# Kernel tuning notes

Hardware: AMD Instinct MI355X
Metric: run time of the kernel (lower is better)

## Reference

```python
import jax, jax.numpy as jnp
import numpy as np

# ---- constants mirroring the torch module ----
OSAMP = 8            # temporal oversampling factor
MAX_ITER = 10        # forward solver iterations (LBFGS replaced by fixed GD)
NEG_SHIFT = 2 * OSAMP
OTP = 5              # baseline frames subtracted from ctc/aif
C_SHARP = 500.0      # sharpness constant C=500 in fermi_ir_func
LR = 0.1             # fixed step size for the deterministic forward solve


def interp_linear_1d(x, size):
    # interp_linear_1D: linear upsampling along last (time) axis
    return jax.image.resize(x, x.shape[:-1] + (size,), method='linear')


def fermi_ir(eta, t_os):
    # eta: [B,3,H,W] = (amplitude A, decay rate k, delay t0); t_os: [Tos]
    tsh = t_os - t_os[NEG_SHIFT]                    # negative time shift
    A = eta[:, 0][..., None]                        # [B,H,W,1]
    k = eta[:, 1][..., None]
    t0 = eta[:, 2][..., None]
    step = jax.nn.sigmoid(C_SHARP * tsh)            # sharp causal onset (C=500)
    return A * jax.nn.sigmoid(k * (t0 - tsh)) * step  # [B,H,W,Tos]


def convolve(aif, ir):
    # linear convolution along time via FFT; output aligned with neg_shift offset
    Tos = ir.shape[-1]
    n = 2 * Tos
    Fa = jnp.fft.rfft(aif, n=n, axis=-1)            # [B,1,1,n/2+1]
    Fi = jnp.fft.rfft(ir, n=n, axis=-1)             # [B,H,W,n/2+1]
    full = jnp.fft.irfft(Fa * Fi, n=n, axis=-1)
    return jax.lax.dynamic_slice_in_dim(full, NEG_SHIFT, Tos, axis=-1)


def make_objective(ctc, aif, time, eta_prior, lambda_reg):
    # preprocessing from FermiDataConsLBFGS.forward
    aif = aif - aif[..., :OTP].mean(-1, keepdims=True)
    ctc = ctc - ctc[..., :OTP].mean(-1, keepdims=True)
    Tos = OSAMP * ctc.shape[-1]
    aif_os = interp_linear_1d(aif, Tos)
    ctc_os = interp_linear_1d(ctc, Tos)
    t_os = interp_linear_1d(time, Tos)
    ctc_dc = ctc_os[..., ::OSAMP]                   # [B,H,W,T]
    C_nn = (eta_prior ** 2).sum(axis=(0, 2, 3), keepdims=True)  # [1,3,1,1]
    C_dc = (ctc_dc ** 2).sum()
    sp_lam = jax.nn.softplus(lambda_reg).squeeze()

    def F_obj(eta):  # FermiDConsObj.__call__ (OD disabled: indx_dc = all frames)
        ir = fermi_ir(eta, t_os)
        ctc_est = convolve(aif_os, ir)[..., ::OSAMP] / OSAMP
        dc = ((ctc_dc - ctc_est) ** 2 / C_dc).sum()
        reg = sp_lam * (((eta - eta_prior) ** 2) / C_nn).sum()
        pos = (jax.nn.relu(-eta) ** 2).sum()
        return dc + reg + pos
    return F_obj


def setup_inputs():
    key = jax.random.key(0)
    k1, k2, k3, k4 = jax.random.split(key, 4)
    B, H, W, T = 1, 128, 128, 64
    ctc = jax.random.normal(k1, (B, H, W, T), jnp.float32) * 0.1
    aif = jax.random.uniform(k2, (B, 1, 1, T), jnp.float32)
    time = jnp.arange(T, dtype=jnp.float32)
    seg = jnp.ones((B, H, W), jnp.int32)
    eta_nn = jax.random.uniform(k3, (B, 3, H, W), jnp.float32)
    lambda_reg = jax.random.normal(k4, (1,), jnp.float32)
    return {"ctc": ctc, "aif": aif, "time": time, "seg": seg,
            "eta_nn": eta_nn, "lambda_reg": lambda_reg}


def reference(ctc, aif, time, seg, eta_nn, lambda_reg):
    # seg only affects the (disabled) outlier-detection path
    F_obj = make_objective(ctc, aif, time, eta_nn, lambda_reg)
    gradF = jax.grad(F_obj)

    def step(eta, _):
        return eta - LR * gradF(eta), None

    eta_pi, _ = jax.lax.scan(step, eta_nn, None, length=MAX_ITER)
    return eta_pi
```

## Files before the change

kernel.cpp:

```cpp
#include <hip/hip_runtime.h>
#include <math.h>

#define T_IN 64
#define NPIX 16384
#define MAX_ITER 10
#define NSLOT 43

typedef _Float16 half8_t __attribute__((ext_vector_type(8)));
typedef __fp16   fp16x2  __attribute__((ext_vector_type(2)));
typedef float    f32x4   __attribute__((ext_vector_type(4)));
typedef int      i32x4   __attribute__((ext_vector_type(4)));

union H8 { half8_t v; fp16x2 h2[4]; i32x4 i4; };

__device__ __forceinline__ float rcp_fast(float x) { return __builtin_amdgcn_rcpf(x); }

__constant__ constexpr int NTMIN[16] = {0,0,0,0,0,1,1,1,1,2,2,2,2,3,3,3};
__constant__ constexpr int TOFS[16]  = {0,4,8,12,16,20,23,26,29,32,34,36,38,40,41,42};

template<int KT>
__device__ __forceinline__ void buildTile(float T0, float nK, float r, int q,
        const float (&d10b)[16], const float (&tse0)[8], const float (&tse15)[8],
        H8& F0h, H8& F1h, H8& F2h) {
    float  x[8];
    fp16x2 d1h[4];
    float  d10 = T0 - d10b[KT];
    const fp16x2 c1 = {(__fp16)0.25f, (__fp16)0.25f};
    const fp16x2 c2 = {(__fp16)0.50f, (__fp16)0.50f};
    const fp16x2 c3 = {(__fp16)0.75f, (__fp16)0.75f};
    bool arith = true;
    if constexpr (KT == 0 || KT == 15) {
        bool flat = (KT == 0) ? (q == 0) : (q == 3);
        if (flat) {
            arith = false;
            const float* te;
            if constexpr (KT == 0) te = tse0; else te = tse15;
            #pragma unroll
            for (int j = 0; j < 8; ++j) x[j] = __expf(nK * (T0 - te[j]));
            #pragma unroll
            for (int jj = 0; jj < 4; ++jj)
                d1h[jj] = __builtin_amdgcn_cvt_pkrtz(T0 - te[2*jj],
                                                     T0 - te[2*jj+1]);
        }
    }
    if (arith) {
        x[0] = __expf(nK * d10);
        x[4] = __expf(nK * (d10 - 0.5f));
        x[1] = x[0]*r; x[2] = x[1]*r; x[3] = x[2]*r;
        x[5] = x[4]*r; x[6] = x[5]*r; x[7] = x[6]*r;
        fp16x2 D0 = __builtin_amdgcn_cvt_pkrtz(d10, d10 - 0.125f);
        d1h[0] = D0;
        d1h[1] = D0 - c1;
        d1h[2] = D0 - c2;
        d1h[3] = D0 - c3;
    }
    #pragma unroll
    for (int jj = 0; jj < 4; ++jj) {
        float s1a = rcp_fast(1.0f + x[2*jj]);
        float s1b = rcp_fast(1.0f + x[2*jj+1]);
        fp16x2 sh = __builtin_amdgcn_cvt_pkrtz(s1a, s1b);
        fp16x2 eh = sh - sh*sh;
        F0h.h2[jj] = sh;
        F1h.h2[jj] = eh * d1h[jj];
        F2h.h2[jj] = eh;
    }
}

template<int KT>
struct Pipe2 {
    static __device__ __forceinline__ void run(float T0, float nK, float r, int q, int lane,
            const float (&d10b)[16], const float (&tse0)[8], const float (&tse15)[8],
            const i32x4* __restrict__ Bs,
            H8 (&F0p)[2], H8 (&F1p)[2], H8 (&F2p)[2],
            f32x4 (&acc)[3][4]) {
        constexpr int PB = (KT >> 1) & 1;
        if constexpr (KT + 2 < 16)
            buildTile<KT+2>(T0, nK, r, q, d10b, tse0, tse15,
                            F0p[PB^1], F1p[PB^1], F2p[PB^1]);
        const f32x4 Z = (f32x4){0.f, 0.f, 0.f, 0.f};
        #pragma unroll
        for (int nt = NTMIN[KT]; nt < 4; ++nt) {
            int slot = TOFS[KT] + nt - NTMIN[KT];
            H8 bh; bh.i4 = Bs[slot*64 + lane];
            if constexpr (KT < 2) {
                acc[0][nt] = __builtin_amdgcn_mfma_f32_16x16x32_f16(F0p[PB].v, bh.v, Z, 0, 0, 0);
                acc[1][nt] = __builtin_amdgcn_mfma_f32_16x16x32_f16(F1p[PB].v, bh.v, Z, 0, 0, 0);
                acc[2][nt] = __builtin_amdgcn_mfma_f32_16x16x32_f16(F2p[PB].v, bh.v, Z, 0, 0, 0);
            } else {
                acc[0][nt] = __builtin_amdgcn_mfma_f32_16x16x32_f16(F0p[PB].v, bh.v, acc[0][nt], 0, 0, 0);
                acc[1][nt] = __builtin_amdgcn_mfma_f32_16x16x32_f16(F1p[PB].v, bh.v, acc[1][nt], 0, 0, 0);
                acc[2][nt] = __builtin_amdgcn_mfma_f32_16x16x32_f16(F2p[PB].v, bh.v, acc[2][nt], 0, 0, 0);
            }
        }
        if constexpr (KT + 2 < 16)
            Pipe2<KT+2>::run(T0, nK, r, q, lane, d10b, tse0, tse15, Bs, F0p, F1p, F2p, acc);
    }
};

template<int H>
__device__ __forceinline__ void pipeAcc(float T0, float nK, float r, int q, int lane,
        const float (&d10b)[16], const float (&tse0)[8], const float (&tse15)[8],
        const i32x4* __restrict__ Bs, f32x4 (&acc)[3][4]) {
    H8 F0p[2], F1p[2], F2p[2];
    buildTile<H>(T0, nK, r, q, d10b, tse0, tse15, F0p[0], F1p[0], F2p[0]);
    Pipe2<H>::run(T0, nK, r, q, lane, d10b, tse0, tse15, Bs, F0p, F1p, F2p, acc);
}

template<int H>
__device__ __forceinline__ void sendHalf(const f32x4 (&acc)[3][4],
        float2* __restrict__ xch, int pair, int lane) {
    constexpr int SB = 2 - 2*H;
    float2* xw = xch + ((pair*2 + H)*12)*64 + lane;
    #pragma unroll
    for (int i = 0; i < 3; ++i)
        #pragma unroll
        for (int nt = 0; nt < 4; ++nt)
            xw[(i*4+nt)*64] = make_float2(acc[i][nt][SB], acc[i][nt][SB+1]);
}

template<int H>
__device__ __forceinline__ void finishDots(f32x4 (&acc)[3][4],
        const float2* __restrict__ xch, float (&Gtab)[2][16][4],
        int pair, int lane, int q, int n,
        const float (&dch)[4][2], float A) {
    constexpr int KB = 2*H;
    const float2* xr = xch + ((pair*2 + (1-H))*12)*64 + lane;
    #pragma unroll
    for (int i = 0; i < 3; ++i)
        #pragma unroll
        for (int nt = 0; nt < 4; ++nt) {
            float2 v = xr[(i*4+nt)*64];
            acc[i][nt][KB]   += v.x;
            acc[i][nt][KB+1] += v.y;
        }
    float Ap0 = __shfl(A, q*4 + KB);
    float Ap1 = __shfl(A, q*4 + KB + 1);
    float SA0=0.f,SK0=0.f,ST0=0.f, SA1=0.f,SK1=0.f,ST1=0.f;
    #pragma unroll
    for (int nt = 0; nt < 4; ++nt) {
        float Y0 = acc[0][nt][KB], Y1 = acc[1][nt][KB], Y2 = acc[2][nt][KB];
        float rr = fmaf(Ap0, Y0, -dch[nt][0]);
        SA0 = fmaf(rr, Y0, SA0); SK0 = fmaf(rr, Y1, SK0); ST0 = fmaf(rr, Y2, ST0);
        float y0 = acc[0][nt][KB+1], y1 = acc[1][nt][KB+1], y2 = acc[2][nt][KB+1];
        float r2 = fmaf(Ap1, y0, -dch[nt][1]);
        SA1 = fmaf(r2, y0, SA1); SK1 = fmaf(r2, y1, SK1); ST1 = fmaf(r2, y2, ST1);
    }
    #pragma unroll
    for (int m = 1; m < 16; m <<= 1) {
        SA0 += __shfl_xor(SA0, m); SK0 += __shfl_xor(SK0, m); ST0 += __shfl_xor(ST0, m);
        SA1 += __shfl_xor(SA1, m); SK1 += __shfl_xor(SK1, m); ST1 += __shfl_xor(ST1, m);
    }
    if (n == 0) {
        float* g = Gtab[pair][q*4 + KB];
        g[0] = SA0; g[1] = SK0; g[2] = ST0;
    }
    if (n == 1) {
        float* g = Gtab[pair][q*4 + KB + 1];
        g[0] = SA1; g[1] = SK1; g[2] = ST1;
    }
}

__global__ __launch_bounds__(256, 1) void k_prep(
        const float* __restrict__ ctc,  const float* __restrict__ aif,
        const float* __restrict__ timev,const float* __restrict__ eta,
        float* __restrict__ tshg, i32x4* __restrict__ Bg,
        f32x4* __restrict__ partials) {
    __shared__ float tshs[512];
    __shared__ float aifos[512];
    __shared__ float a_s[64], t_s[64];
    __shared__ f32x4 red[4];

    const int tid  = threadIdx.x;
    const int lane = tid & 63;
    const int wid  = tid >> 6;
    const int q = lane >> 4, n = lane & 15;
    const int pixbase = blockIdx.x * 64 + wid * 16;
    const int mypix   = pixbase + n;

    if (tid < 64) { a_s[tid] = aif[tid]; t_s[tid] = timev[tid]; }
    float A  = eta[mypix];
    float K  = eta[NPIX + mypix];
    float T0 = eta[2*NPIX + mypix];
    __syncthreads();
    {
        float m5a = 0.2f * (a_s[0]+a_s[1]+a_s[2]+a_s[3]+a_s[4]);
        float t16;
        {
            float xx = 1.5625f; int i0 = (int)xx; float f = xx - (float)i0;
            t16 = t_s[i0]*(1.0f-f) + t_s[i0+1]*f;
        }
        #pragma unroll
        for (int rep = 0; rep < 2; ++rep) {
            int i = tid + 256*rep;
            float x = ((float)i - 3.5f) * 0.125f;
            float ao, to;
            if (x <= 0.0f)       { ao = a_s[0]  - m5a; to = t_s[0];  }
            else if (x >= 63.0f) { ao = a_s[63] - m5a; to = t_s[63]; }
            else {
                int i0 = (int)x; float f = x - (float)i0;
                ao = (a_s[i0]-m5a)*(1.0f-f) + (a_s[i0+1]-m5a)*f;
                to = t_s[i0]*(1.0f-f) + t_s[i0+1]*f;
            }
            aifos[i] = ao;
            tshs[i]  = to - t16;
            if (blockIdx.x == 0) tshg[i] = to - t16;
        }
    }
    __syncthreads();

    if (blockIdx.x < NSLOT && tid < 64) {
        int slot = blockIdx.x, l = tid;
        int kt, nt;
        if (slot < 20)      { kt = slot >> 2; nt = slot & 3; }
        else if (slot < 32) { int s = slot - 20; int d3 = s / 3; kt = 5 + d3; nt = 1 + (s - 3*d3); }
        else if (slot < 40) { int s = slot - 32; kt = 9 + (s >> 1); nt = 2 + (s & 1); }
        else                { kt = 13 + (slot - 40); nt = 3; }
        int kbase = 32*kt + 8*(l >> 4);
        int m = 16 + 8 * (16*nt + (l & 15));
        H8 bh;
        #pragma unroll
        for (int jj = 0; jj < 4; ++jj) {
            float v[2];
            #pragma unroll
            for (int h = 0; h < 2; ++h) {
                int k  = kbase + 2*jj + h;
                int ai = m - k;
                float s2 = 1.0f / (1.0f + __expf(-500.0f * tshs[k]));
                v[h] = (ai >= 0 && ai < 512) ? s2 * aifos[ai] * 0.125f : 0.0f;
            }
            bh.h2[jj] = (fp16x2){(__fp16)v[0], (__fp16)v[1]};
        }
        Bg[slot*64 + l] = bh.i4;
    }

    float vs = 0.f;
    #pragma unroll
    for (int reg = 0; reg < 4; ++reg) {
        const float* cp = ctc + (pixbase + q*4 + reg) * T_IN;
        float m5 = 0.2f * (cp[0]+cp[1]+cp[2]+cp[3]+cp[4]);
        #pragma unroll
        for (int nt = 0; nt < 4; ++nt) {
            int d = nt*16 + n;
            float cc = cp[d] - m5;
            float cm = cp[(d > 0) ? d-1 : 0] - m5;
            float dc = (d == 0) ? cc : (0.4375f*cm + 0.5625f*cc);
            vs += dc * dc;
        }
    }
    {
        f32x4 pv = (f32x4){vs, 0.25f*A*A, 0.25f*K*K, 0.25f*T0*T0};
        #pragma unroll
        for (int m = 1; m < 64; m <<= 1) {
            pv.x += __shfl_xor(pv.x, m); pv.y += __shfl_xor(pv.y, m);
            pv.z += __shfl_xor(pv.z, m); pv.w += __shfl_xor(pv.w, m);
        }
        if (lane == 0) red[wid] = pv;
    }
    __syncthreads();
    if (tid == 0)
        partials[blockIdx.x] = red[0] + red[1] + red[2] + red[3];
}

__global__ __launch_bounds__(256, 2) void k_iter(
        const float* __restrict__ ctc,  const float* __restrict__ lam,
        const float* __restrict__ eta,  const float* __restrict__ tshg,
        const i32x4* __restrict__ Bg,   const f32x4* __restrict__ partials,
        float* __restrict__ out) {
    __shared__ i32x4 Bs[NSLOT * 64];
    __shared__ float tshs[512];
    __shared__ float2 xch[2*2*12*64];
    __shared__ float Gtab[2][16][4];

    const int tid  = threadIdx.x;
    const int lane = tid & 63;
    const int wid  = tid >> 6;
    const int hh   = wid & 1;
    const int pair = wid >> 1;
    const int q = lane >> 4, n = lane & 15;
    const int pixbase = blockIdx.x * 32 + pair * 16;
    const int mypix   = pixbase + n;

    for (int idx = tid; idx < NSLOT * 64; idx += 256) Bs[idx] = Bg[idx];
    tshs[tid] = tshg[tid];
    tshs[tid + 256] = tshg[tid + 256];

    float A  = eta[mypix];
    float K  = eta[NPIX + mypix];
    float T0 = eta[2*NPIX + mypix];
    const float pA = A, pK = K, pT = T0;

    float dch[4][2];
    #pragma unroll
    for (int j = 0; j < 2; ++j) {
        const float* cp = ctc + (pixbase + q*4 + 2*hh + j) * T_IN;
        float m5 = 0.2f * (cp[0]+cp[1]+cp[2]+cp[3]+cp[4]);
        #pragma unroll
        for (int nt = 0; nt < 4; ++nt) {
            int d = nt*16 + n;
            float cc = cp[d] - m5;
            float cm = cp[(d > 0) ? d-1 : 0] - m5;
            dch[nt][j] = (d == 0) ? cc : (0.4375f*cm + 0.5625f*cc);
        }
    }

    f32x4 tot = partials[lane] + partials[64+lane] + partials[128+lane]
              + partials[192+lane];
    #pragma unroll
    for (int m = 1; m < 64; m <<= 1) {
        tot.x += __shfl_xor(tot.x, m); tot.y += __shfl_xor(tot.y, m);
        tot.z += __shfl_xor(tot.z, m); tot.w += __shfl_xor(tot.w, m);
    }
    float spl;
    {
        float xl = lam[0];
        spl = (xl > 0.0f) ? (xl + log1pf(__expf(-xl))) : log1pf(__expf(xl));
    }
    const float cdc2 = 2.0f / tot.x;
    const float rgA  = 2.0f * spl / tot.y;
    const float rgK  = 2.0f * spl / tot.z;
    const float rgT  = 2.0f * spl / tot.w;

    __syncthreads();

    float  d10b[16];
    float  tse0[8], tse15[8];
    #pragma unroll
    for (int kt = 0; kt < 16; ++kt) d10b[kt] = tshs[32*kt + 8*q];
    #pragma unroll
    for (int j = 0; j < 8; ++j) { tse0[j] = tshs[8*q + j]; tse15[j] = tshs[480 + 8*q + j]; }

    #pragma unroll 1
    for (int it = 0; it < MAX_ITER; ++it) {
        float nK = -K;
        float r  = __expf(0.125f * K);

        f32x4 acc[3][4];
        if (hh == 0) {
            pipeAcc<0>(T0, nK, r, q, lane, d10b, tse0, tse15, Bs, acc);
            sendHalf<0>(acc, xch, pair, lane);
        } else {
            pipeAcc<1>(T0, nK, r, q, lane, d10b, tse0, tse15, Bs, acc);
            sendHalf<1>(acc, xch, pair, lane);
        }
        __syncthreads();
        if (hh == 0) finishDots<0>(acc, xch, Gtab, pair, lane, q, n, dch, A);
        else         finishDots<1>(acc, xch, Gtab, pair, lane, q, n, dch, A);
        __syncthreads();

        const float GA = Gtab[pair][n][0];
        const float GK = Gtab[pair][n][1];
        const float GT = Gtab[pair][n][2];
        float gA = fmaf(rgA, A  - pA, cdc2 * GA)         + 2.0f * fminf(A,  0.f);
        float gK = fmaf(rgK, K  - pK, cdc2 * A * GK)     + 2.0f * fminf(K,  0.f);
        float gT = fmaf(rgT, T0 - pT, cdc2 * A * K * GT) + 2.0f * fminf(T0, 0.f);
        A  -= 0.1f * gA;
        K  -= 0.1f * gK;
        T0 -= 0.1f * gT;
    }

    if (hh == 0 && lane < 16) {
        out[mypix]          = A;
        out[NPIX + mypix]   = K;
        out[2*NPIX + mypix] = T0;
    }
}

extern "C" void kernel_launch(void* const* d_in, const int* in_sizes, int n_in,
                              void* d_out, int out_size, void* d_ws, size_t ws_size,
                              hipStream_t stream) {
    const float* ctc   = (const float*)d_in[0];
    const float* aif   = (const float*)d_in[1];
    const float* timev = (const float*)d_in[2];
    const float* eta   = (const float*)d_in[4];
    const float* lam   = (const float*)d_in[5];
    float* out = (float*)d_out;
    f32x4* partials = (f32x4*)d_ws;
    float* tshg     = (float*)((char*)d_ws + 4096);
    i32x4* Bg       = (i32x4*)((char*)d_ws + 8192);

    k_prep<<<NPIX / 64, 256, 0, stream>>>(ctc, aif, timev, eta,
                                          tshg, Bg, partials);
    k_iter<<<NPIX / 32, 256, 0, stream>>>(ctc, lam, eta, tshg, Bg,
                                          partials, out);
}
```

Measured before the change: 106.0 us.

## Hold Toeplitz B fragments in registers instead of LDS per iteration

Each wave now loads only the B-matrix fragments its half (even or odd K tiles) needs, straight from global memory into a 23-entry register array, once before the iteration loop. The MFMA loop reads operands from registers instead of LDS every iteration, and the LDS staging copy, the tsh table and one __syncthreads go away. Per-wave time constants are trimmed to only the entries each half uses. This costs about 92 extra VGPRs per lane, which under launch_bounds(256,2) may cause spills or lower occupancy.

```diff
diff --git a/kernel.cpp b/kernel.cpp
--- a/kernel.cpp
+++ b/kernel.cpp
@@ -17,14 +17,16 @@
 
 __constant__ constexpr int NTMIN[16] = {0,0,0,0,0,1,1,1,1,2,2,2,2,3,3,3};
 __constant__ constexpr int TOFS[16]  = {0,4,8,12,16,20,23,26,29,32,34,36,38,40,41,42};
+__constant__ constexpr int POS[16]   = {0,0,4,4,8,8,12,11,15,14,18,16,20,18,22,19};
+#define NBREG 23
 
 template<int KT>
 __device__ __forceinline__ void buildTile(float T0, float nK, float r, int q,
-        const float (&d10b)[16], const float (&tse0)[8], const float (&tse15)[8],
+        const float (&d10s)[8], const float (&tse)[8],
         H8& F0h, H8& F1h, H8& F2h) {
     float  x[8];
     fp16x2 d1h[4];
-    float  d10 = T0 - d10b[KT];
+    float  d10 = T0 - d10s[KT >> 1];
     const fp16x2 c1 = {(__fp16)0.25f, (__fp16)0.25f};
     const fp16x2 c2 = {(__fp16)0.50f, (__fp16)0.50f};
     const fp16x2 c3 = {(__fp16)0.75f, (__fp16)0.75f};
@@ -33,14 +35,12 @@
         bool flat = (KT == 0) ? (q == 0) : (q == 3);
         if (flat) {
             arith = false;
-            const float* te;
-            if constexpr (KT == 0) te = tse0; else te = tse15;
             #pragma unroll
-            for (int j = 0; j < 8; ++j) x[j] = __expf(nK * (T0 - te[j]));
+            for (int j = 0; j < 8; ++j) x[j] = __expf(nK * (T0 - tse[j]));
             #pragma unroll
             for (int jj = 0; jj < 4; ++jj)
-                d1h[jj] = __builtin_amdgcn_cvt_pkrtz(T0 - te[2*jj],
-                                                     T0 - te[2*jj+1]);
+                d1h[jj] = __builtin_amdgcn_cvt_pkrtz(T0 - tse[2*jj],
+                                                     T0 - tse[2*jj+1]);
         }
     }
     if (arith) {
@@ -66,45 +66,70 @@
     }
 }
 
+template<int KT, int NT, int PB>
+struct MfmaNT {
+    static __device__ __forceinline__ void run(const i32x4 (&Breg)[NBREG],
+            const H8 (&F0p)[2], const H8 (&F1p)[2], const H8 (&F2p)[2],
+            f32x4 (&acc)[3][4]) {
+        constexpr int idx = POS[KT] + NT - NTMIN[KT];
+        H8 bh; bh.i4 = Breg[idx];
+        if constexpr (KT < 2) {
+            const f32x4 Z = (f32x4){0.f, 0.f, 0.f, 0.f};
+            acc[0][NT] = __builtin_amdgcn_mfma_f32_16x16x32_f16(F0p[PB].v, bh.v, Z, 0, 0, 0);
+            acc[1][NT] = __builtin_amdgcn_mfma_f32_16x16x32_f16(F1p[PB].v, bh.v, Z, 0, 0, 0);
+            acc[2][NT] = __builtin_amdgcn_mfma_f32_16x16x32_f16(F2p[PB].v, bh.v, Z, 0, 0, 0);
+        } else {
+            acc[0][NT] = __builtin_amdgcn_mfma_f32_16x16x32_f16(F0p[PB].v, bh.v, acc[0][NT], 0, 0, 0);
+            acc[1][NT] = __builtin_amdgcn_mfma_f32_16x16x32_f16(F1p[PB].v, bh.v, acc[1][NT], 0, 0, 0);
+            acc[2][NT] = __builtin_amdgcn_mfma_f32_16x16x32_f16(F2p[PB].v, bh.v, acc[2][NT], 0, 0, 0);
+        }
+        if constexpr (NT + 1 < 4)
+            MfmaNT<KT, NT+1, PB>::run(Breg, F0p, F1p, F2p, acc);
+    }
+};
+
 template<int KT>
-struct Pipe2 {
-    static __device__ __forceinline__ void run(float T0, float nK, float r, int q, int lane,
-            const float (&d10b)[16], const float (&tse0)[8], const float (&tse15)[8],
-            const i32x4* __restrict__ Bs,
+struct Pipe2R {
+    static __device__ __forceinline__ void run(float T0, float nK, float r, int q,
+            const float (&d10s)[8], const float (&tse)[8],
+            const i32x4 (&Breg)[NBREG],
             H8 (&F0p)[2], H8 (&F1p)[2], H8 (&F2p)[2],
             f32x4 (&acc)[3][4]) {
         constexpr int PB = (KT >> 1) & 1;
         if constexpr (KT + 2 < 16)
-            buildTile<KT+2>(T0, nK, r, q, d10b, tse0, tse15,
+            buildTile<KT+2>(T0, nK, r, q, d10s, tse,
                             F0p[PB^1], F1p[PB^1], F2p[PB^1]);
-        const f32x4 Z = (f32x4){0.f, 0.f, 0.f, 0.f};
-        #pragma unroll
-        for (int nt = NTMIN[KT]; nt < 4; ++nt) {
-            int slot = TOFS[KT] + nt - NTMIN[KT];
-            H8 bh; bh.i4 = Bs[slot*64 + lane];
-            if constexpr (KT < 2) {
-                acc[0][nt] = __builtin_amdgcn_mfma_f32_16x16x32_f16(F0p[PB].v, bh.v, Z, 0, 0, 0);
-                acc[1][nt] = __builtin_amdgcn_mfma_f32_16x16x32_f16(F1p[PB].v, bh.v, Z, 0, 0, 0);
-                acc[2][nt] = __builtin_amdgcn_mfma_f32_16x16x32_f16(F2p[PB].v, bh.v, Z, 0, 0, 0);
-            } else {
-                acc[0][nt] = __builtin_amdgcn_mfma_f32_16x16x32_f16(F0p[PB].v, bh.v, acc[0][nt], 0, 0, 0);
-                acc[1][nt] = __builtin_amdgcn_mfma_f32_16x16x32_f16(F1p[PB].v, bh.v, acc[1][nt], 0, 0, 0);
-                acc[2][nt] = __builtin_amdgcn_mfma_f32_16x16x32_f16(F2p[PB].v, bh.v, acc[2][nt], 0, 0, 0);
-            }
-        }
+        MfmaNT<KT, NTMIN[KT], PB>::run(Breg, F0p, F1p, F2p, acc);
         if constexpr (KT + 2 < 16)
-            Pipe2<KT+2>::run(T0, nK, r, q, lane, d10b, tse0, tse15, Bs, F0p, F1p, F2p, acc);
+            Pipe2R<KT+2>::run(T0, nK, r, q, d10s, tse, Breg, F0p, F1p, F2p, acc);
     }
 };
 
 template<int H>
-__device__ __forceinline__ void pipeAcc(float T0, float nK, float r, int q, int lane,
-        const float (&d10b)[16], const float (&tse0)[8], const float (&tse15)[8],
-        const i32x4* __restrict__ Bs, f32x4 (&acc)[3][4]) {
+__device__ __forceinline__ void pipeAcc(float T0, float nK, float r, int q,
+        const float (&d10s)[8], const float (&tse)[8],
+        const i32x4 (&Breg)[NBREG], f32x4 (&acc)[3][4]) {
     H8 F0p[2], F1p[2], F2p[2];
-    buildTile<H>(T0, nK, r, q, d10b, tse0, tse15, F0p[0], F1p[0], F2p[0]);
-    Pipe2<H>::run(T0, nK, r, q, lane, d10b, tse0, tse15, Bs, F0p, F1p, F2p, acc);
-}
+    buildTile<H>(T0, nK, r, q, d10s, tse, F0p[0], F1p[0], F2p[0]);
+    Pipe2R<H>::run(T0, nK, r, q, d10s, tse, Breg, F0p, F1p, F2p, acc);
+}
+
+template<int KT, int NT>
+struct LoadNT {
+    static __device__ __forceinline__ void run(const i32x4* __restrict__ Bgl,
+                                               i32x4 (&Breg)[NBREG]) {
+        Breg[POS[KT] + NT - NTMIN[KT]] = Bgl[(TOFS[KT] + NT - NTMIN[KT]) * 64];
+        if constexpr (NT + 1 < 4) LoadNT<KT, NT+1>::run(Bgl, Breg);
+    }
+};
+template<int KT>
+struct LoadB {
+    static __device__ __forceinline__ void run(const i32x4* __restrict__ Bgl,
+                                               i32x4 (&Breg)[NBREG]) {
+        LoadNT<KT, NTMIN[KT]>::run(Bgl, Breg);
+        if constexpr (KT + 2 < 16) LoadB<KT+2>::run(Bgl, Breg);
+    }
+};
 
 template<int H>
 __device__ __forceinline__ void sendHalf(const f32x4 (&acc)[3][4],
@@ -266,8 +291,6 @@
         const float* __restrict__ eta,  const float* __restrict__ tshg,
         const i32x4* __restrict__ Bg,   const f32x4* __restrict__ partials,
         float* __restrict__ out) {
-    __shared__ i32x4 Bs[NSLOT * 64];
-    __shared__ float tshs[512];
     __shared__ float2 xch[2*2*12*64];
     __shared__ float Gtab[2][16][4];
 
@@ -280,9 +303,10 @@
     const int pixbase = blockIdx.x * 32 + pair * 16;
     const int mypix   = pixbase + n;
 
-    for (int idx = tid; idx < NSLOT * 64; idx += 256) Bs[idx] = Bg[idx];
-    tshs[tid] = tshg[tid];
-    tshs[tid + 256] = tshg[tid + 256];
+    const i32x4* Bgl = Bg + lane;
+    i32x4 Breg[NBREG];
+    if (hh == 0) LoadB<0>::run(Bgl, Breg);
+    else         LoadB<1>::run(Bgl, Breg);
 
     float A  = eta[mypix];
     float K  = eta[NPIX + mypix];
@@ -303,6 +327,16 @@
         }
     }
 
+    float d10s[8];
+    #pragma unroll
+    for (int j = 0; j < 8; ++j) d10s[j] = tshg[32*(2*j + hh) + 8*q];
+    float tse[8];
+    {
+        const float* tb = hh ? (tshg + 480) : tshg;
+        #pragma unroll
+        for (int j = 0; j < 8; ++j) tse[j] = tb[8*q + j];
+    }
+
     f32x4 tot = partials[lane] + partials[64+lane] + partials[128+lane]
               + partials[192+lane];
     #pragma unroll
@@ -320,15 +354,6 @@
     const float rgK  = 2.0f * spl / tot.z;
     const float rgT  = 2.0f * spl / tot.w;
 
-    __syncthreads();
-
-    float  d10b[16];
-    float  tse0[8], tse15[8];
-    #pragma unroll
-    for (int kt = 0; kt < 16; ++kt) d10b[kt] = tshs[32*kt + 8*q];
-    #pragma unroll
-    for (int j = 0; j < 8; ++j) { tse0[j] = tshs[8*q + j]; tse15[j] = tshs[480 + 8*q + j]; }
-
     #pragma unroll 1
     for (int it = 0; it < MAX_ITER; ++it) {
         float nK = -K;
@@ -336,10 +361,10 @@
 
         f32x4 acc[3][4];
         if (hh == 0) {
-            pipeAcc<0>(T0, nK, r, q, lane, d10b, tse0, tse15, Bs, acc);
+            pipeAcc<0>(T0, nK, r, q, d10s, tse, Breg, acc);
             sendHalf<0>(acc, xch, pair, lane);
         } else {
-            pipeAcc<1>(T0, nK, r, q, lane, d10b, tse0, tse15, Bs, acc);
+            pipeAcc<1>(T0, nK, r, q, d10s, tse, Breg, acc);
             sendHalf<1>(acc, xch, pair, lane);
         }
         __syncthreads();
```

Result: no change. 104.0 us (-1.9%).
